# Kernel optimization log

Hardware: AMD Instinct MI355X
Metric: run time of the kernel (lower is better)

Reference implementation:

```python
import jax, jax.numpy as jnp
import numpy as np

W_BITS = 8
A_BITS = 8


def sym_quant(x, num_bits):
    # Symmetric per-last-dim abs-max quantization (SymQuantizer.forward, ndim<=3,
    # layerwise=False): s = (2^(b-1)-1)/(max|x| + 1e-6); q = round(x*s)/(s+1e-6)
    max_abs = jnp.max(jnp.abs(x), axis=-1, keepdims=True)
    s = (2.0 ** (num_bits - 1) - 1.0) / (max_abs + 1e-6)
    return jnp.round(x * s) / (s + 1e-6)


def setup_inputs() -> dict:
    key = jax.random.key(0)
    kx, kw = jax.random.split(key)
    B, S, NX, NF = 4, 2048, 1600, 6400
    x = jax.random.normal(kx, (B, S, NX), dtype=jnp.float32)
    weight = 0.02 * jax.random.normal(kw, (NX, NF), dtype=jnp.float32)  # Conv1D: [nx, nf]
    bias = jnp.zeros((NF,), dtype=jnp.float32)
    return {"x": x, "weight": weight, "bias": bias}


def reference(x, weight, bias):
    # quantize weights per-row (over nf), quantize activations per-token (over nx)
    wq = sym_quant(weight, W_BITS)
    xq = sym_quant(x, A_BITS)
    # addmm(bias, x.view(-1, nx), weight) then reshape back
    return jnp.einsum("bsx,xf->bsf", xq, wq) + bias
```

## Files before the change

kernel.cpp:

```cpp
#include <hip/hip_runtime.h>
#include <stdint.h>

typedef _Float16 f16;
typedef _Float16 f16x4 __attribute__((ext_vector_type(4)));
typedef _Float16 f16x8 __attribute__((ext_vector_type(8)));
typedef float f32x4 __attribute__((ext_vector_type(4)));

#define K_DIM 1600
#define NF_DIM 6400
#define KPAD 1664
#define NKT 26
#define KPB (KPAD * 2)

__device__ __forceinline__ void async_copy16(const void* g, void* l) {
    __builtin_amdgcn_global_load_lds(
        (const __attribute__((address_space(1))) void*)(uintptr_t)g,
        (__attribute__((address_space(3))) void*)(uint32_t)(uintptr_t)l,
        16, 0, 0);
}

__device__ __forceinline__ float blockMax(float v, float* sm) {
#pragma unroll
    for (int off = 32; off > 0; off >>= 1)
        v = fmaxf(v, __shfl_down(v, off, 64));
    int wid = threadIdx.x >> 6, lane = threadIdx.x & 63;
    if (lane == 0) sm[wid] = v;
    __syncthreads();
    if (threadIdx.x == 0) {
        float m = sm[0];
        for (int i = 1; i < (int)(blockDim.x >> 6); ++i) m = fmaxf(m, sm[i]);
        sm[0] = m;
    }
    __syncthreads();
    return sm[0];
}

__global__ void quant_x_kernel(const float* __restrict__ x, f16* __restrict__ qx,
                               float* __restrict__ ax) {
    __shared__ float sm[4];
    size_t row = blockIdx.x;
    const float* xr = x + row * (size_t)K_DIM;
    float m = 0.f;
    const int n4 = K_DIM >> 2;
    for (int i = threadIdx.x; i < n4; i += blockDim.x) {
        float4 v = ((const float4*)xr)[i];
        m = fmaxf(fmaxf(fmaxf(fabsf(v.x), fabsf(v.y)), fmaxf(fabsf(v.z), fabsf(v.w))), m);
    }
    m = blockMax(m, sm);
    float s = 127.0f / (m + 1e-6f);
    if (threadIdx.x == 0) ax[row] = 1.0f / (s + 1e-6f);
    f16* qr = qx + row * (size_t)KPAD;
    for (int i = threadIdx.x; i < n4; i += blockDim.x) {
        float4 v = ((const float4*)xr)[i];
        f16x4 q;
        q[0] = (f16)rintf(v.x * s);
        q[1] = (f16)rintf(v.y * s);
        q[2] = (f16)rintf(v.z * s);
        q[3] = (f16)rintf(v.w * s);
        *(f16x4*)&qr[i * 4] = q;
    }
    if (threadIdx.x < 16) {
        f16x4 z = {};
        *(f16x4*)&qr[K_DIM + threadIdx.x * 4] = z;
    }
}

__global__ void wscale_kernel(const float* __restrict__ w, float* __restrict__ sw) {
    __shared__ float sm[4];
    size_t k = blockIdx.x;
    const float* wr = w + k * (size_t)NF_DIM;
    float m = 0.f;
    const int n4 = NF_DIM >> 2;
    for (int i = threadIdx.x; i < n4; i += blockDim.x) {
        float4 v = ((const float4*)wr)[i];
        m = fmaxf(fmaxf(fmaxf(fabsf(v.x), fabsf(v.y)), fmaxf(fabsf(v.z), fabsf(v.w))), m);
    }
    m = blockMax(m, sm);
    if (threadIdx.x == 0) sw[k] = 127.0f / (m + 1e-6f);
}

__global__ void wtq_kernel(const float* __restrict__ w, const float* __restrict__ sw,
                           f16* __restrict__ wqt) {
    __shared__ f16 t[64][80];
    int k0 = blockIdx.x * 64;
    int f0 = blockIdx.y * 64;
    int tid = threadIdx.x;
    if (k0 >= K_DIM) {
        int fr = tid >> 2;
        int ch = (tid & 3) << 4;
        float4 z = {};
        float4* dst = (float4*)&wqt[(size_t)(f0 + fr) * KPAD + k0 + ch];
        dst[0] = z;
        dst[1] = z;
        return;
    }
    int rr = tid >> 4;
    int cc = (tid & 15) << 2;
#pragma unroll
    for (int i = 0; i < 4; ++i) {
        int r = rr + i * 16;
        float s = sw[k0 + r];
        float inv = 1.0f / (s + 1e-6f);
        float4 v = *(const float4*)&w[(size_t)(k0 + r) * NF_DIM + f0 + cc];
        t[cc + 0][r] = (f16)(rintf(v.x * s) * inv);
        t[cc + 1][r] = (f16)(rintf(v.y * s) * inv);
        t[cc + 2][r] = (f16)(rintf(v.z * s) * inv);
        t[cc + 3][r] = (f16)(rintf(v.w * s) * inv);
    }
    __syncthreads();
    int fr = tid >> 2;
    int ch = (tid & 3) << 4;
    const float4* src = (const float4*)&t[fr][ch];
    float4* dst = (float4*)&wqt[(size_t)(f0 + fr) * KPAD + k0 + ch];
    dst[0] = src[0];
    dst[1] = src[1];
}

__global__ __launch_bounds__(512, 1) void gemm256(
    const f16* __restrict__ A,
    const f16* __restrict__ Bt,
    const float* __restrict__ ax,
    const float* __restrict__ bias,
    float* __restrict__ C, int M, int N) {
    extern __shared__ char lds[];

    const int tid = threadIdx.x;
    const int lane = tid & 63;
    const int wv = tid >> 6;
    const int wm = wv >> 2;
    const int wn = wv & 3;
    const int lr = lane & 15;
    const int lg = lane >> 4;

    const int nTn = N / 256;
    const int bid = blockIdx.x;
    const int cpx = gridDim.x >> 3;
    const int swz = (bid & 7) * cpx + (bid >> 3);
    const int tm = swz / nTn, tn = swz % nTn;
    const size_t m0 = (size_t)tm * 256, n0 = (size_t)tn * 256;

    const int srow8 = lane >> 3;
    const int sslot = (lane & 7) ^ srow8;
    const char* pAlo = (const char*)A + (m0 + (size_t)(wv * 16 + srow8)) * KPB + sslot * 16;
    const char* pAhi = pAlo + (size_t)128 * KPB;
    const char* pBlo = (const char*)Bt + (n0 + (size_t)(wv * 16 + srow8)) * KPB + sslot * 16;
    const char* pBhi = pBlo + (size_t)128 * KPB;
    const int L0 = wv * 2048 + lane * 16;

#define ST(gp, t, roff)                                       \
    {                                                         \
        const char* g_ = (gp) + (size_t)(t) * 128;            \
        async_copy16(g_, lds + (roff) + L0);                  \
        async_copy16(g_ + 8 * KPB, lds + (roff) + L0 + 1024); \
    }

    const int swz0 = ((lg) ^ (lr & 7)) << 4;
    const int swz1 = ((4 + lg) ^ (lr & 7)) << 4;
    const int rbA = (wm * 128 + lr) * 128;
    const int rbB = 32768 + (wn * 64 + lr) * 128;

#define RD_ALO(bsel)                                                 \
    {                                                                \
        const char* p0_ = lds + (bsel) + rbA + swz0;                 \
        const char* p1_ = lds + (bsel) + rbA + swz1;                 \
        _Pragma("unroll") for (int mi_ = 0; mi_ < 4; ++mi_) {        \
            alo[mi_][0] = *(const f16x8*)(p0_ + mi_ * 2048);         \
            alo[mi_][1] = *(const f16x8*)(p1_ + mi_ * 2048);         \
        }                                                            \
    }
#define RD_AHI(bsel)                                                 \
    {                                                                \
        const char* p0_ = lds + (bsel) + rbA + swz0 + 8192;          \
        const char* p1_ = lds + (bsel) + rbA + swz1 + 8192;          \
        _Pragma("unroll") for (int mi_ = 0; mi_ < 4; ++mi_) {        \
            ahi[mi_][0] = *(const f16x8*)(p0_ + mi_ * 2048);         \
            ahi[mi_][1] = *(const f16x8*)(p1_ + mi_ * 2048);         \
        }                                                            \
    }
#define RD_BLO(bsel)                                                 \
    {                                                                \
        const char* p0_ = lds + (bsel) + rbB + swz0;                 \
        const char* p1_ = lds + (bsel) + rbB + swz1;                 \
        _Pragma("unroll") for (int ni_ = 0; ni_ < 2; ++ni_) {        \
            blo[ni_][0] = *(const f16x8*)(p0_ + ni_ * 2048);         \
            blo[ni_][1] = *(const f16x8*)(p1_ + ni_ * 2048);         \
        }                                                            \
    }
#define RD_BHI(bsel)                                                 \
    {                                                                \
        const char* p0_ = lds + (bsel) + rbB + swz0 + 4096;          \
        const char* p1_ = lds + (bsel) + rbB + swz1 + 4096;          \
        _Pragma("unroll") for (int ni_ = 0; ni_ < 2; ++ni_) {        \
            bhi[ni_][0] = *(const f16x8*)(p0_ + ni_ * 2048);         \
            bhi[ni_][1] = *(const f16x8*)(p1_ + ni_ * 2048);         \
        }                                                            \
    }

#define BARRIER __builtin_amdgcn_s_barrier()
#define LGKM(n) asm volatile("s_waitcnt lgkmcnt(" #n ")" ::: "memory")
#define SB0 __builtin_amdgcn_sched_barrier(0)
#define VM4 asm volatile("s_waitcnt vmcnt(4)" ::: "memory")

#define MF(AF, BF, R0, C0)                                                        \
    {                                                                             \
        __builtin_amdgcn_s_setprio(1);                                            \
        _Pragma("unroll") for (int mi_ = 0; mi_ < 4; ++mi_)                       \
        _Pragma("unroll") for (int ni_ = 0; ni_ < 2; ++ni_)                       \
        _Pragma("unroll") for (int kk_ = 0; kk_ < 2; ++kk_)                       \
            acc[(R0) + mi_][(C0) + ni_] = __builtin_amdgcn_mfma_f32_16x16x32_f16( \
                AF[mi_][kk_], BF[ni_][kk_], acc[(R0) + mi_][(C0) + ni_], 0, 0, 0);\
        __builtin_amdgcn_s_setprio(0);                                            \
    }

    f32x4 acc[8][4] = {};
    f16x8 alo[4][2], ahi[4][2], blo[2][2], bhi[2][2];
    const int b0 = 0, b1 = 65536;

    ST(pAlo, 0, b0 + 0);
    ST(pAhi, 0, b0 + 16384);
    ST(pBlo, 0, b0 + 32768);
    ST(pBhi, 0, b0 + 49152);
    ST(pBlo, 1, b1 + 32768);
    ST(pBhi, 1, b1 + 49152);
    VM4;
    BARRIER;
    RD_ALO(b0);
    RD_BLO(b0);

    for (int i = 0; i < NKT / 2; ++i) {
        const int t1s = 2 * i + 1;
        const int tp2 = (2 * i + 2 < NKT) ? 2 * i + 2 : NKT - 1;
        const int tp3 = (2 * i + 3 < NKT) ? 2 * i + 3 : NKT - 1;

        RD_BHI(b0);
        ST(pAlo, t1s, b1 + 0);
        BARRIER; LGKM(4); SB0;
        MF(alo, blo, 0, 0);
        BARRIER;

        RD_AHI(b0);
        ST(pAhi, t1s, b1 + 16384);
        BARRIER; LGKM(8); SB0;
        MF(alo, bhi, 0, 2);
        BARRIER;

        ST(pBlo, tp2, b0 + 32768);
        BARRIER; LGKM(0); SB0;
        MF(ahi, blo, 4, 0);
        BARRIER;

        ST(pBhi, tp2, b0 + 49152);
        VM4;
        BARRIER;
        RD_ALO(b1);
        RD_BLO(b1);
        SB0;
        MF(ahi, bhi, 4, 2);
        BARRIER;

        RD_BHI(b1);
        ST(pAlo, tp2, b0 + 0);
        BARRIER; LGKM(4); SB0;
        MF(alo, blo, 0, 0);
        BARRIER;

        RD_AHI(b1);
        ST(pAhi, tp2, b0 + 16384);
        BARRIER; LGKM(8); SB0;
        MF(alo, bhi, 0, 2);
        BARRIER;

        ST(pBlo, tp3, b1 + 32768);
        BARRIER; LGKM(0); SB0;
        MF(ahi, blo, 4, 0);
        BARRIER;

        ST(pBhi, tp3, b1 + 49152);
        VM4;
        BARRIER;
        RD_ALO(b0);
        RD_BLO(b0);
        SB0;
        MF(ahi, bhi, 4, 2);
        BARRIER;
    }
    asm volatile("s_waitcnt vmcnt(0) lgkmcnt(0)" ::: "memory");
    __syncthreads();

    const float4 b4 = *(const float4*)&bias[n0 + lane * 4];
    float* wbase = (float*)lds + wv * 1088;
#pragma unroll
    for (int mi = 0; mi < 8; ++mi) {
        __syncthreads();
#pragma unroll
        for (int ni = 0; ni < 4; ++ni)
#pragma unroll
            for (int j = 0; j < 4; ++j)
                wbase[(lg * 4 + j) * 68 + ni * 16 + lr] = acc[mi][ni][j];
        __syncthreads();
#pragma unroll
        for (int k = 0; k < 4; ++k) {
            int rr = wv * 4 + k;
            int wmp = rr >> 4, r16 = rr & 15;
            size_t mg = m0 + wmp * 128 + mi * 16 + r16;
            float axv = ax[mg];
            int wvp = wmp * 4 + (lane >> 4);
            float4 v = *(const float4*)((const float*)lds + wvp * 1088 + r16 * 68 + (lane & 15) * 4);
            float4 o;
            o.x = v.x * axv + b4.x;
            o.y = v.y * axv + b4.y;
            o.z = v.z * axv + b4.z;
            o.w = v.w * axv + b4.w;
            *(float4*)&C[mg * (size_t)N + n0 + lane * 4] = o;
        }
    }
}

extern "C" void kernel_launch(void* const* d_in, const int* in_sizes, int n_in,
                              void* d_out, int out_size, void* d_ws, size_t ws_size,
                              hipStream_t stream) {
    const float* x = (const float*)d_in[0];
    const float* w = (const float*)d_in[1];
    const float* bias = (const float*)d_in[2];
    float* out = (float*)d_out;

    const int M = in_sizes[0] / K_DIM;
    const int N = NF_DIM;

    char* ws = (char*)d_ws;
    f16* qx = (f16*)ws;
    f16* wqt = (f16*)(ws + (size_t)M * KPAD * 2);
    float* ax = (float*)(ws + (size_t)M * KPAD * 2 + (size_t)N * KPAD * 2);
    float* sw = ax + M;

    quant_x_kernel<<<M, 256, 0, stream>>>(x, qx, ax);
    wscale_kernel<<<K_DIM, 256, 0, stream>>>(w, sw);
    wtq_kernel<<<dim3(KPAD / 64, NF_DIM / 64), 256, 0, stream>>>(w, sw, wqt);

    (void)hipFuncSetAttribute((const void*)gemm256,
                              hipFuncAttributeMaxDynamicSharedMemorySize, 131072);
    gemm256<<<(M / 256) * (N / 256), 512, 131072, stream>>>(qx, wqt, ax, bias, out, M, N);
}
```

Baseline: 254.5 us.

## Reorder MFMA inner loop to split K halves instead of N halves per phase

Restructures the LDS fragment reads and MFMA phases so each phase covers one 16-element K slice across all four N sub-tiles, rather than one N half across both K slices. A and B fragments for the two K halves are double-buffered in registers (aA/aB, b0/b1), and the lgkmcnt waits are adjusted so LDS reads overlap the previous phase's MFMAs. The aim is more even interleaving of LDS reads with matrix ops and fewer full lgkmcnt(0) stalls. The register footprint and wait counts change, which risks spills or wrong waits.

```diff
diff --git a/kernel.cpp b/kernel.cpp
--- a/kernel.cpp
+++ b/kernel.cpp
@@ -159,41 +159,19 @@
     const int rbA = (wm * 128 + lr) * 128;
     const int rbB = 32768 + (wn * 64 + lr) * 128;
 
-#define RD_ALO(bsel)                                                 \
-    {                                                                \
-        const char* p0_ = lds + (bsel) + rbA + swz0;                 \
-        const char* p1_ = lds + (bsel) + rbA + swz1;                 \
-        _Pragma("unroll") for (int mi_ = 0; mi_ < 4; ++mi_) {        \
-            alo[mi_][0] = *(const f16x8*)(p0_ + mi_ * 2048);         \
-            alo[mi_][1] = *(const f16x8*)(p1_ + mi_ * 2048);         \
-        }                                                            \
-    }
-#define RD_AHI(bsel)                                                 \
-    {                                                                \
-        const char* p0_ = lds + (bsel) + rbA + swz0 + 8192;          \
-        const char* p1_ = lds + (bsel) + rbA + swz1 + 8192;          \
-        _Pragma("unroll") for (int mi_ = 0; mi_ < 4; ++mi_) {        \
-            ahi[mi_][0] = *(const f16x8*)(p0_ + mi_ * 2048);         \
-            ahi[mi_][1] = *(const f16x8*)(p1_ + mi_ * 2048);         \
-        }                                                            \
-    }
-#define RD_BLO(bsel)                                                 \
-    {                                                                \
-        const char* p0_ = lds + (bsel) + rbB + swz0;                 \
-        const char* p1_ = lds + (bsel) + rbB + swz1;                 \
-        _Pragma("unroll") for (int ni_ = 0; ni_ < 2; ++ni_) {        \
-            blo[ni_][0] = *(const f16x8*)(p0_ + ni_ * 2048);         \
-            blo[ni_][1] = *(const f16x8*)(p1_ + ni_ * 2048);         \
-        }                                                            \
-    }
-#define RD_BHI(bsel)                                                 \
-    {                                                                \
-        const char* p0_ = lds + (bsel) + rbB + swz0 + 4096;          \
-        const char* p1_ = lds + (bsel) + rbB + swz1 + 4096;          \
-        _Pragma("unroll") for (int ni_ = 0; ni_ < 2; ++ni_) {        \
-            bhi[ni_][0] = *(const f16x8*)(p0_ + ni_ * 2048);         \
-            bhi[ni_][1] = *(const f16x8*)(p1_ + ni_ * 2048);         \
-        }                                                            \
+#define RD_A(dst, bsel, rowoff, sz)                                     \
+    {                                                                   \
+        const char* p_ = lds + (bsel) + rbA + (rowoff) + (sz);          \
+        _Pragma("unroll") for (int mi_ = 0; mi_ < 4; ++mi_)             \
+            dst[mi_] = *(const f16x8*)(p_ + mi_ * 2048);                \
+    }
+#define RD_B(dlo, dhi, bsel, sz)                                        \
+    {                                                                   \
+        const char* p_ = lds + (bsel) + rbB + (sz);                     \
+        _Pragma("unroll") for (int ni_ = 0; ni_ < 2; ++ni_) {           \
+            dlo[ni_] = *(const f16x8*)(p_ + ni_ * 2048);                \
+            dhi[ni_] = *(const f16x8*)(p_ + 4096 + ni_ * 2048);         \
+        }                                                               \
     }
 
 #define BARRIER __builtin_amdgcn_s_barrier()
@@ -201,19 +179,24 @@
 #define SB0 __builtin_amdgcn_sched_barrier(0)
 #define VM4 asm volatile("s_waitcnt vmcnt(4)" ::: "memory")
 
-#define MF(AF, BF, R0, C0)                                                        \
+#define MFC(AF, BL, BH, MOFF)                                                     \
     {                                                                             \
         __builtin_amdgcn_s_setprio(1);                                            \
-        _Pragma("unroll") for (int mi_ = 0; mi_ < 4; ++mi_)                       \
-        _Pragma("unroll") for (int ni_ = 0; ni_ < 2; ++ni_)                       \
-        _Pragma("unroll") for (int kk_ = 0; kk_ < 2; ++kk_)                       \
-            acc[(R0) + mi_][(C0) + ni_] = __builtin_amdgcn_mfma_f32_16x16x32_f16( \
-                AF[mi_][kk_], BF[ni_][kk_], acc[(R0) + mi_][(C0) + ni_], 0, 0, 0);\
+        _Pragma("unroll") for (int mi_ = 0; mi_ < 4; ++mi_) {                     \
+            _Pragma("unroll") for (int ni_ = 0; ni_ < 2; ++ni_) {                 \
+                acc[(MOFF) + mi_][ni_] = __builtin_amdgcn_mfma_f32_16x16x32_f16(  \
+                    AF[mi_], BL[ni_], acc[(MOFF) + mi_][ni_], 0, 0, 0);           \
+                acc[(MOFF) + mi_][2 + ni_] = __builtin_amdgcn_mfma_f32_16x16x32_f16( \
+                    AF[mi_], BH[ni_], acc[(MOFF) + mi_][2 + ni_], 0, 0, 0);       \
+            }                                                                     \
+        }                                                                         \
         __builtin_amdgcn_s_setprio(0);                                            \
     }
 
     f32x4 acc[8][4] = {};
-    f16x8 alo[4][2], ahi[4][2], blo[2][2], bhi[2][2];
+    f16x8 aA[4], aB[4];
+    f16x8 b0lo[2], b0hi[2];
+    f16x8 b1lo[2], b1hi[2];
     const int b0 = 0, b1 = 65536;
 
     ST(pAlo, 0, b0 + 0);
@@ -224,64 +207,68 @@
     ST(pBhi, 1, b1 + 49152);
     VM4;
     BARRIER;
-    RD_ALO(b0);
-    RD_BLO(b0);
+    RD_A(aA, b0, 0, swz0);
+    RD_B(b0lo, b0hi, b0, swz0);
 
     for (int i = 0; i < NKT / 2; ++i) {
         const int t1s = 2 * i + 1;
         const int tp2 = (2 * i + 2 < NKT) ? 2 * i + 2 : NKT - 1;
         const int tp3 = (2 * i + 3 < NKT) ? 2 * i + 3 : NKT - 1;
 
-        RD_BHI(b0);
+        RD_A(aB, b0, 0, swz1);
+        RD_B(b1lo, b1hi, b0, swz1);
         ST(pAlo, t1s, b1 + 0);
+        BARRIER; LGKM(8); SB0;
+        MFC(aA, b0lo, b0hi, 0);
+        BARRIER;
+
+        RD_A(aA, b0, 8192, swz0);
+        ST(pAhi, t1s, b1 + 16384);
         BARRIER; LGKM(4); SB0;
-        MF(alo, blo, 0, 0);
-        BARRIER;
-
-        RD_AHI(b0);
-        ST(pAhi, t1s, b1 + 16384);
-        BARRIER; LGKM(8); SB0;
-        MF(alo, bhi, 0, 2);
-        BARRIER;
-
+        MFC(aB, b1lo, b1hi, 0);
+        BARRIER;
+
+        RD_A(aB, b0, 8192, swz1);
         ST(pBlo, tp2, b0 + 32768);
-        BARRIER; LGKM(0); SB0;
-        MF(ahi, blo, 4, 0);
+        BARRIER; LGKM(4); SB0;
+        MFC(aA, b0lo, b0hi, 4);
         BARRIER;
 
         ST(pBhi, tp2, b0 + 49152);
         VM4;
         BARRIER;
-        RD_ALO(b1);
-        RD_BLO(b1);
-        SB0;
-        MF(ahi, bhi, 4, 2);
-        BARRIER;
-
-        RD_BHI(b1);
+        RD_A(aA, b1, 0, swz0);
+        RD_B(b0lo, b0hi, b1, swz0);
+        LGKM(8); SB0;
+        MFC(aB, b1lo, b1hi, 4);
+        BARRIER;
+
+        RD_A(aB, b1, 0, swz1);
+        RD_B(b1lo, b1hi, b1, swz1);
         ST(pAlo, tp2, b0 + 0);
+        BARRIER; LGKM(8); SB0;
+        MFC(aA, b0lo, b0hi, 0);
+        BARRIER;
+
+        RD_A(aA, b1, 8192, swz0);
+        ST(pAhi, tp2, b0 + 16384);
         BARRIER; LGKM(4); SB0;
-        MF(alo, blo, 0, 0);
-        BARRIER;
-
-        RD_AHI(b1);
-        ST(pAhi, tp2, b0 + 16384);
-        BARRIER; LGKM(8); SB0;
-        MF(alo, bhi, 0, 2);
-        BARRIER;
-
+        MFC(aB, b1lo, b1hi, 0);
+        BARRIER;
+
+        RD_A(aB, b1, 8192, swz1);
         ST(pBlo, tp3, b1 + 32768);
-        BARRIER; LGKM(0); SB0;
-        MF(ahi, blo, 4, 0);
+        BARRIER; LGKM(4); SB0;
+        MFC(aA, b0lo, b0hi, 4);
         BARRIER;
 
         ST(pBhi, tp3, b1 + 49152);
         VM4;
         BARRIER;
-        RD_ALO(b0);
-        RD_BLO(b0);
-        SB0;
-        MF(ahi, bhi, 4, 2);
+        RD_A(aA, b0, 0, swz0);
+        RD_B(b0lo, b0hi, b0, swz0);
+        LGKM(8); SB0;
+        MFC(aB, b1lo, b1hi, 4);
         BARRIER;
     }
     asm volatile("s_waitcnt vmcnt(0) lgkmcnt(0)" ::: "memory");
```

After: 237.8 us. 1.07x faster.
